# Optimization experiments

Hardware: AMD Instinct MI355X
Metric: run time of the kernel (lower is better)

## Reference

```python
import jax, jax.numpy as jnp
import numpy as np

N_USERS = 100000
N_ITEMS = 50000
N_NODES = N_USERS + N_ITEMS
N_EDGES = 4800000
EMB = 64
N_LAYERS = 3
BATCH = 16384


def setup_inputs() -> dict:
    key = jax.random.key(0)
    ks = jax.random.split(key, 12)
    users = jax.random.randint(ks[0], (BATCH,), 0, N_USERS)
    pos_items = jax.random.randint(ks[1], (BATCH,), 0, N_ITEMS)
    neg_items = jax.random.randint(ks[2], (BATCH,), 0, N_ITEMS)
    rows = jax.random.randint(ks[3], (N_EDGES,), 0, N_NODES)
    cols = jax.random.randint(ks[4], (N_EDGES,), 0, N_NODES)
    vals = jax.random.uniform(ks[5], (N_EDGES,), dtype=jnp.float32)
    # learned parameters (xavier-ish scale)
    user_emb = jax.random.normal(ks[6], (N_USERS, EMB), dtype=jnp.float32) * 0.1
    item_emb = jax.random.normal(ks[7], (N_ITEMS, EMB), dtype=jnp.float32) * 0.1
    # Linear weights stored as [in, out] so y = x @ W + b (matches torch Linear math)
    W1s = jax.random.normal(ks[8], (N_LAYERS, EMB, EMB), dtype=jnp.float32) * (1.0 / np.sqrt(EMB))
    b1s = jnp.zeros((N_LAYERS, EMB), dtype=jnp.float32)
    W2s = jax.random.normal(ks[9], (N_LAYERS, EMB, EMB), dtype=jnp.float32) * (1.0 / np.sqrt(EMB))
    b2s = jnp.zeros((N_LAYERS, EMB), dtype=jnp.float32)
    return dict(users=users, pos_items=pos_items, neg_items=neg_items,
                rows=rows, cols=cols, vals=vals,
                user_emb=user_emb, item_emb=item_emb,
                W1s=W1s, b1s=b1s, W2s=W2s, b2s=b2s)


def _leaky_relu(x):
    return jnp.where(x > 0, x, 0.2 * x)


def _computer(user_emb, item_emb, rows, cols, vals, W1s, b1s, W2s, b2s):
    all_emb = jnp.concatenate([user_emb, item_emb], axis=0)  # [N, 64]
    embs = [all_emb]
    for i in range(N_LAYERS):
        self_emb = all_emb @ W1s[i] + b1s[i]
        # sparse adjacency SpMM: gather neighbor features, weight, segment-sum by row
        neighbor = jax.ops.segment_sum(vals[:, None] * all_emb[cols], rows,
                                       num_segments=N_NODES)
        neighbor = neighbor @ W2s[i] + b2s[i]
        interact = (neighbor * all_emb) @ W2s[i] + b2s[i]
        all_emb = _leaky_relu(self_emb + neighbor + interact)
        embs.append(all_emb)
    embs = jnp.concatenate(embs, axis=1)  # [N, 64*(n_layers+1)] = [N, 256]
    return embs[:N_USERS], embs[N_USERS:]


def reference(users, pos_items, neg_items, rows, cols, vals,
              user_emb, item_emb, W1s, b1s, W2s, b2s):
    all_users, all_items = _computer(user_emb, item_emb, rows, cols, vals,
                                     W1s, b1s, W2s, b2s)
    users_emb = all_users[users]
    pos_emb = all_items[pos_items]
    neg_emb = all_items[neg_items]
    return users_emb, pos_emb, neg_emb
```

## Files before the change

kernel.cpp:

```cpp
#include <hip/hip_runtime.h>


#define EMB 64

constexpr int kNUsers = 100000;
constexpr int kNItems = 50000;
constexpr int kNNodes = 150000;
constexpr int kNEdges = 4800000;
constexpr int kBatch  = 16384;
constexpr int kLayers = 3;
constexpr int kRngShift = 8;
constexpr int kNRanges  = (kNNodes + 255) >> 8;
constexpr int kEdgesPerBin = 16384;
constexpr int kBinBlocks = (kNEdges + kEdgesPerBin - 1) / kEdgesPerBin;
constexpr int kEPW    = 16;

__device__ __forceinline__ float f4c(const float4& v, int i) {
  return ((const float*)&v)[i];
}
__device__ __forceinline__ float4 f4fma(float s, float4 w, float4 a) {
  a.x = fmaf(s, w.x, a.x);
  a.y = fmaf(s, w.y, a.y);
  a.z = fmaf(s, w.z, a.z);
  a.w = fmaf(s, w.w, a.w);
  return a;
}
__device__ __forceinline__ float4 f4add(float4 a, float4 b) {
  a.x += b.x; a.y += b.y; a.z += b.z; a.w += b.w;
  return a;
}
__device__ __forceinline__ float lrelu(float x) { return x > 0.f ? x : 0.2f * x; }
__device__ __forceinline__ unsigned short f2bf(float f) {
  unsigned int u = __float_as_uint(f);
  u = (u + 0x7fffu + ((u >> 16) & 1u)) >> 16;
  return (unsigned short)u;
}
__device__ __forceinline__ float bf2f(unsigned short h) {
  return __uint_as_float(((unsigned int)h) << 16);
}

#define F16(M) M(0) M(1) M(2) M(3) M(4) M(5) M(6) M(7) \
               M(8) M(9) M(10) M(11) M(12) M(13) M(14) M(15)

__global__ __launch_bounds__(256) void init_embed(
    const float* __restrict__ user_emb, const float* __restrict__ item_emb,
    float* __restrict__ cur, unsigned short* __restrict__ cur16, int with16)
{
  const size_t userF = (size_t)kNUsers * EMB;
  const size_t allF4 = (size_t)kNNodes * EMB / 4;
  const size_t i = (size_t)blockIdx.x * 256 + threadIdx.x;
  if (i >= allF4) return;
  const size_t f = i * 4;
  const float4 v = (f < userF) ? ((const float4*)user_emb)[i]
                               : ((const float4*)(item_emb))[(f - userF) / 4];
  ((float4*)cur)[i] = v;
  if (with16) {
    ushort4 h;
    h.x = f2bf(v.x); h.y = f2bf(v.y); h.z = f2bf(v.z); h.w = f2bf(v.w);
    ((ushort4*)cur16)[i] = h;
  }
}

__global__ __launch_bounds__(256) void refresh16(
    const float* __restrict__ cur, unsigned short* __restrict__ cur16)
{
  const size_t allF4 = (size_t)kNNodes * EMB / 4;
  const size_t i = (size_t)blockIdx.x * 256 + threadIdx.x;
  if (i >= allF4) return;
  const float4 v = ((const float4*)cur)[i];
  ushort4 h;
  h.x = f2bf(v.x); h.y = f2bf(v.y); h.z = f2bf(v.z); h.w = f2bf(v.w);
  ((ushort4*)cur16)[i] = h;
}


__global__ __launch_bounds__(1024) void hist_ranges(
    const int* __restrict__ rows, int* __restrict__ rangeA)
{
  __shared__ int cnt[kNRanges];
  const int tid = threadIdx.x;
  const int e0  = blockIdx.x * kEdgesPerBin;
  int e1 = e0 + kEdgesPerBin;
  if (e1 > kNEdges) e1 = kNEdges;
  for (int b = tid; b < kNRanges; b += 1024) cnt[b] = 0;
  __syncthreads();
  for (int e = e0 + tid; e < e1; e += 1024)
    atomicAdd(&cnt[rows[e] >> kRngShift], 1);
  __syncthreads();
  for (int b = tid; b < kNRanges; b += 1024)
    if (cnt[b] > 0) atomicAdd(&rangeA[b], cnt[b]);
}

__global__ __launch_bounds__(1024) void scan_ranges(
    int* __restrict__ rangeA, int* __restrict__ rowPtr)
{
  __shared__ int wsum[16];
  const int tid  = threadIdx.x;
  const int lane = tid & 63;
  const int wid  = tid >> 6;
  const int cnt  = (tid < kNRanges) ? rangeA[tid] : 0;
  int v = cnt;
#pragma unroll
  for (int off = 1; off < 64; off <<= 1) {
    const int n = __shfl_up(v, off, 64);
    if (lane >= off) v += n;
  }
  if (lane == 63) wsum[wid] = v;
  __syncthreads();
  if (tid == 0) {
    int s = 0;
#pragma unroll
    for (int w = 0; w < 16; ++w) { const int t = wsum[w]; wsum[w] = s; s += t; }
  }
  __syncthreads();
  if (tid < kNRanges) rangeA[tid] = wsum[wid] + v - cnt;
  if (tid == 0) {
    rangeA[kNRanges]  = kNEdges;
    rowPtr[kNNodes]   = kNEdges;
  }
}

__global__ __launch_bounds__(1024) void bin_edges(
    const int* __restrict__ rows, const int* __restrict__ cols,
    const float* __restrict__ vals, const int* __restrict__ rangeA,
    int* __restrict__ rangeCnt, int2* __restrict__ tmpE)
{
  __shared__ int cnt[kNRanges];
  __shared__ int base[kNRanges];
  const int tid = threadIdx.x;
  const int e0  = blockIdx.x * kEdgesPerBin;
  int e1 = e0 + kEdgesPerBin;
  if (e1 > kNEdges) e1 = kNEdges;

  for (int b = tid; b < kNRanges; b += 1024) cnt[b] = 0;
  __syncthreads();
  for (int e = e0 + tid; e < e1; e += 1024)
    atomicAdd(&cnt[rows[e] >> kRngShift], 1);
  __syncthreads();
  for (int b = tid; b < kNRanges; b += 1024) {
    const int c = cnt[b];
    base[b] = (c > 0) ? (rangeA[b] + atomicAdd(&rangeCnt[b], c)) : 0;
    cnt[b] = 0;
  }
  __syncthreads();
  for (int e = e0 + tid; e < e1; e += 1024) {
    const int r = rows[e];
    const int b = r >> kRngShift;
    const int rank = atomicAdd(&cnt[b], 1);
    tmpE[base[b] + rank] =
        make_int2(cols[e] | ((r & 255) << 18), __float_as_int(vals[e]));
  }
}

__global__ __launch_bounds__(256) void place_edges(
    const int2* __restrict__ tmpE, const int* __restrict__ rangeA,
    int2* __restrict__ edgeS, int* __restrict__ rowPtr)
{
  __shared__ int lcnt[256];
  __shared__ int lbase[256];
  __shared__ int ws[4];
  const int b    = blockIdx.x;
  const int r0   = b << kRngShift;
  const int tid  = threadIdx.x;
  const int lane = tid & 63;
  const int wid  = tid >> 6;
  const int start = rangeA[b];
  const int end   = rangeA[b + 1];

  lcnt[tid] = 0;
  __syncthreads();
  for (int e = start + tid; e < end; e += 256)
    atomicAdd(&lcnt[(tmpE[e].x >> 18) & 255], 1);
  __syncthreads();

  const int c = lcnt[tid];
  int v = c;
#pragma unroll
  for (int off = 1; off < 64; off <<= 1) {
    const int n = __shfl_up(v, off, 64);
    if (lane >= off) v += n;
  }
  if (lane == 63) ws[wid] = v;
  __syncthreads();
  int wadd = 0;
#pragma unroll
  for (int w = 0; w < 4; ++w) if (w < wid) wadd += ws[w];
  const int excl = v - c + wadd;
  lbase[tid] = start + excl;
  if (r0 + tid < kNNodes) rowPtr[r0 + tid] = start + excl;
  lcnt[tid] = 0;
  __syncthreads();

  for (int e = start + tid; e < end; e += 256) {
    const int2 cv = tmpE[e];
    const int rl  = (cv.x >> 18) & 255;
    const int rank = atomicAdd(&lcnt[rl], 1);
    edgeS[lbase[rl] + rank] = make_int2(cv.x & 0x3FFFF, cv.y);
  }
}

__global__ __launch_bounds__(256) void spmm_csr16f(
    const unsigned short* __restrict__ cur16, const int* __restrict__ rowPtr,
    const int2* __restrict__ edgeS, const float* __restrict__ W2,
    const float* __restrict__ b2, float* __restrict__ nbuf)
{
  const int lane = threadIdx.x & 63;
  const int r = (blockIdx.x << 2) | (threadIdx.x >> 6);
  if (r >= kNNodes) return;
  const int start = __builtin_amdgcn_readfirstlane(rowPtr[r]);
  const int end   = __builtin_amdgcn_readfirstlane(rowPtr[r + 1]);
  float a0 = 0.f, a1 = 0.f, a2 = 0.f, a3 = 0.f;
  int e = start;
  for (; e + 4 <= end; e += 4) {
    const int2 cv0 = edgeS[e];
    const int2 cv1 = edgeS[e + 1];
    const int2 cv2 = edgeS[e + 2];
    const int2 cv3 = edgeS[e + 3];
    const unsigned short u0 = cur16[(size_t)cv0.x * EMB + lane];
    const unsigned short u1 = cur16[(size_t)cv1.x * EMB + lane];
    const unsigned short u2 = cur16[(size_t)cv2.x * EMB + lane];
    const unsigned short u3 = cur16[(size_t)cv3.x * EMB + lane];
    a0 = fmaf(__int_as_float(cv0.y), bf2f(u0), a0);
    a1 = fmaf(__int_as_float(cv1.y), bf2f(u1), a1);
    a2 = fmaf(__int_as_float(cv2.y), bf2f(u2), a2);
    a3 = fmaf(__int_as_float(cv3.y), bf2f(u3), a3);
  }
  for (; e < end; ++e) {
    const int2 cv = edgeS[e];
    a0 = fmaf(__int_as_float(cv.y), bf2f(cur16[(size_t)cv.x * EMB + lane]), a0);
  }
  const float nsum = (a0 + a1) + (a2 + a3);

  float t = b2[lane];
#pragma unroll
  for (int k = 0; k < 64; ++k) {
    const float nk = __shfl(nsum, k, 64);
    t = fmaf(nk, W2[k * EMB + lane], t);
  }
  nbuf[(size_t)r * EMB + lane] = t;
}

__global__ __launch_bounds__(256) void spmm_csr(
    const float* __restrict__ cur, const int* __restrict__ rowPtr,
    const int2* __restrict__ edgeS, float* __restrict__ nbuf)
{
  const int lane = threadIdx.x & 63;
  const int r = (blockIdx.x << 2) | (threadIdx.x >> 6);
  if (r >= kNNodes) return;
  const int start = __builtin_amdgcn_readfirstlane(rowPtr[r]);
  const int end   = __builtin_amdgcn_readfirstlane(rowPtr[r + 1]);
  float a0 = 0.f, a1 = 0.f, a2 = 0.f, a3 = 0.f;
  int e = start;
  for (; e + 4 <= end; e += 4) {
    const int2 cv0 = edgeS[e];
    const int2 cv1 = edgeS[e + 1];
    const int2 cv2 = edgeS[e + 2];
    const int2 cv3 = edgeS[e + 3];
    a0 = fmaf(__int_as_float(cv0.y), cur[(size_t)cv0.x * EMB + lane], a0);
    a1 = fmaf(__int_as_float(cv1.y), cur[(size_t)cv1.x * EMB + lane], a1);
    a2 = fmaf(__int_as_float(cv2.y), cur[(size_t)cv2.x * EMB + lane], a2);
    a3 = fmaf(__int_as_float(cv3.y), cur[(size_t)cv3.x * EMB + lane], a3);
  }
  for (; e < end; ++e) {
    const int2 cv = edgeS[e];
    a0 = fmaf(__int_as_float(cv.y), cur[(size_t)cv.x * EMB + lane], a0);
  }
  nbuf[(size_t)r * EMB + lane] = (a0 + a1) + (a2 + a3);
}

__global__ __launch_bounds__(256) void spmm_atomic(
    const float* __restrict__ cur, const int* __restrict__ rows,
    const int* __restrict__ cols, const float* __restrict__ vals,
    float* __restrict__ nbuf)
{
  const int lane = threadIdx.x & 63;
  int wv = (blockIdx.x << 2) | (threadIdx.x >> 6);
  wv = __builtin_amdgcn_readfirstlane(wv);
  int e0 = wv * kEPW;
  int e1 = e0 + kEPW;
  if (e1 > kNEdges) e1 = kNEdges;
  for (int e = e0; e < e1; ++e) {
    atomicAdd(nbuf + (size_t)rows[e] * EMB + lane,
              vals[e] * cur[(size_t)cols[e] * EMB + lane]);
  }
}

__global__ __launch_bounds__(256) void transform_nbr(
    float* __restrict__ nbuf, const float* __restrict__ W2,
    const float* __restrict__ b2)
{
  const int node = blockIdx.x * 256 + threadIdx.x;
  if (node >= kNNodes) return;
  const float4* __restrict__ nr  = (const float4*)(nbuf + (size_t)node * EMB);
  const float4* __restrict__ b2v = (const float4*)b2;
#define DECL(j) float4 a##j = b2v[j];
  F16(DECL)
#undef DECL
#pragma unroll 4
  for (int k4 = 0; k4 < 16; ++k4) {
    const float4 nv = nr[k4];
#pragma unroll
    for (int kk = 0; kk < 4; ++kk) {
      const float ns = f4c(nv, kk);
      const float4* __restrict__ w2r = (const float4*)(W2 + (4 * k4 + kk) * EMB);
#define STEP(j) a##j = f4fma(ns, w2r[j], a##j);
      F16(STEP)
#undef STEP
    }
  }
  float4* __restrict__ outp = (float4*)(nbuf + (size_t)node * EMB);
#define STORE(j) outp[j] = a##j;
  F16(STORE)
#undef STORE
}

__global__ __launch_bounds__(256) void transform_self(
    float* __restrict__ cur, const float* __restrict__ nbuf,
    const float* __restrict__ W1, const float* __restrict__ b1,
    const float* __restrict__ b2, const float* __restrict__ W2)
{
  const int node = blockIdx.x * 256 + threadIdx.x;
  if (node >= kNNodes) return;
  const float4* __restrict__ xr  = (const float4*)(cur  + (size_t)node * EMB);
  const float4* __restrict__ tr  = (const float4*)(nbuf + (size_t)node * EMB);
  const float4* __restrict__ b1v = (const float4*)b1;
  const float4* __restrict__ b2v = (const float4*)b2;
#define DECL(j) float4 a##j = f4add(b1v[j], b2v[j]);
  F16(DECL)
#undef DECL
#pragma unroll 2
  for (int k4 = 0; k4 < 16; ++k4) {
    const float4 xv = xr[k4];
    const float4 tv = tr[k4];
#pragma unroll
    for (int kk = 0; kk < 4; ++kk) {
      const float xs = f4c(xv, kk);
      const float ms = f4c(tv, kk) * xs;
      const int k = 4 * k4 + kk;
      const float4* __restrict__ w1r = (const float4*)(W1 + k * EMB);
      const float4* __restrict__ w2r = (const float4*)(W2 + k * EMB);
#define STEP(j) a##j = f4fma(xs, w1r[j], a##j); a##j = f4fma(ms, w2r[j], a##j);
      F16(STEP)
#undef STEP
    }
  }
  float4* __restrict__ outp = (float4*)(cur + (size_t)node * EMB);
#define STORE(j) { const float4 tj = tr[j]; float4 r;          \
    r.x = lrelu(a##j.x + tj.x); r.y = lrelu(a##j.y + tj.y);    \
    r.z = lrelu(a##j.z + tj.z); r.w = lrelu(a##j.w + tj.w);    \
    outp[j] = r; }
  F16(STORE)
#undef STORE
}

__global__ __launch_bounds__(256) void gather_out(
    const float* __restrict__ cur, const int* __restrict__ users,
    const int* __restrict__ pos, const int* __restrict__ neg,
    float* __restrict__ out, int layer)
{
  const int t    = blockIdx.x * 256 + threadIdx.x;
  const int lane = t & 63;
  const int rid  = t >> 6;
  if (rid >= 3 * kBatch) return;
  const int seg = rid / kBatch;
  const int b   = rid - seg * kBatch;
  int idx;
  if (seg == 0)      idx = users[b];
  else if (seg == 1) idx = pos[b] + kNUsers;
  else               idx = neg[b] + kNUsers;
  out[(size_t)rid * 256 + layer * EMB + lane] = cur[(size_t)idx * EMB + lane];
}

extern "C" void kernel_launch(void* const* d_in, const int* in_sizes, int n_in,
                              void* d_out, int out_size, void* d_ws, size_t ws_size,
                              hipStream_t stream) {
  const int*   users    = (const int*)d_in[0];
  const int*   pos      = (const int*)d_in[1];
  const int*   neg      = (const int*)d_in[2];
  const int*   rows     = (const int*)d_in[3];
  const int*   cols     = (const int*)d_in[4];
  const float* vals     = (const float*)d_in[5];
  const float* user_emb = (const float*)d_in[6];
  const float* item_emb = (const float*)d_in[7];
  const float* W1s      = (const float*)d_in[8];
  const float* b1s      = (const float*)d_in[9];
  const float* W2s      = (const float*)d_in[10];
  const float* b2s      = (const float*)d_in[11];
  float* out = (float*)d_out;

  const size_t nodeF = (size_t)kNNodes * EMB;
  float* cur  = (float*)d_ws;
  float* nbuf = cur + nodeF;
  int2*  edgeS     = (int2*)(nbuf + nodeF);
  int*   rowPtr    = (int*)(edgeS + kNEdges);
  int*   rangeA    = rowPtr + (kNNodes + 1);
  int*   rangeCnt  = rangeA + (kNRanges + 1);
  unsigned short* cur16 = (unsigned short*)(rangeCnt + kNRanges);
  int2*  tmpE = (int2*)nbuf;
  const size_t neededCsr = (size_t)((char*)cur16 - (char*)d_ws);
  const size_t needed16  = neededCsr + nodeF * sizeof(unsigned short);
  const bool useCsr = ws_size >= neededCsr;
  const bool use16  = useCsr && ws_size >= needed16;

  const dim3 blk(256);
  const int iblocks = (int)((nodeF / 4 + 255) / 256);
  const int gblocks = (3 * kBatch * EMB + 255) / 256;
  const int rblocks = (kNNodes + 3) / 4;
  const int tblocks = (kNNodes + 255) / 256;

  init_embed<<<iblocks, blk, 0, stream>>>(user_emb, item_emb, cur, cur16,
                                          use16 ? 1 : 0);

  if (useCsr) {
    hipMemsetAsync(rangeA, 0, (size_t)(2 * kNRanges + 1) * sizeof(int), stream);
    hist_ranges<<<kBinBlocks, dim3(1024), 0, stream>>>(rows, rangeA);
    scan_ranges<<<1, 1024, 0, stream>>>(rangeA, rowPtr);
    bin_edges<<<kBinBlocks, dim3(1024), 0, stream>>>(rows, cols, vals, rangeA,
                                                     rangeCnt, tmpE);
    place_edges<<<kNRanges, blk, 0, stream>>>(tmpE, rangeA, edgeS, rowPtr);
  }

  gather_out<<<gblocks, blk, 0, stream>>>(cur, users, pos, neg, out, 0);

  for (int L = 0; L < kLayers; ++L) {
    const float* W1 = W1s + L * EMB * EMB;
    const float* b1 = b1s + L * EMB;
    const float* W2 = W2s + L * EMB * EMB;
    const float* b2 = b2s + L * EMB;
    if (useCsr && use16) {
      spmm_csr16f<<<rblocks, blk, 0, stream>>>(cur16, rowPtr, edgeS, W2, b2,
                                               nbuf);
    } else if (useCsr) {
      spmm_csr<<<rblocks, blk, 0, stream>>>(cur, rowPtr, edgeS, nbuf);
      transform_nbr<<<tblocks, blk, 0, stream>>>(nbuf, W2, b2);
    } else {
      hipMemsetAsync(nbuf, 0, nodeF * sizeof(float), stream);
      const int sblocks = (((kNEdges + kEPW - 1) / kEPW) + 3) / 4;
      spmm_atomic<<<sblocks, blk, 0, stream>>>(cur, rows, cols, vals, nbuf);
      transform_nbr<<<tblocks, blk, 0, stream>>>(nbuf, W2, b2);
    }
    transform_self<<<tblocks, blk, 0, stream>>>(cur, nbuf, W1, b1, b2, W2);
    if (use16 && L + 1 < kLayers)
      refresh16<<<iblocks, blk, 0, stream>>>(cur, cur16);
    gather_out<<<gblocks, blk, 0, stream>>>(cur, users, pos, neg, out, L + 1);
  }
}
```

Before: 1.177 ms.

## Stage binned edges in shared memory for coalesced scatter; split W2 accumulator chain

The edge-binning kernel now processes 4096-edge sub-blocks. Each sub-block computes local ranks, prefix-sums the per-range counts, and sorts its records into shared memory, so the writes to tmpE become contiguous runs per range instead of scattered 8-byte stores. This adds shared-memory use and more barriers per sub-block. Separately, the per-row 64x64 W2 product in the fused SpMM kernel now uses four independent accumulators to shorten the FMA dependency chain.

```diff
diff --git a/kernel.cpp b/kernel.cpp
--- a/kernel.cpp
+++ b/kernel.cpp
@@ -13,6 +13,7 @@
 constexpr int kNRanges  = (kNNodes + 255) >> 8;
 constexpr int kEdgesPerBin = 16384;
 constexpr int kBinBlocks = (kNEdges + kEdgesPerBin - 1) / kEdgesPerBin;
+constexpr int kSub    = 4096;
 constexpr int kEPW    = 16;
 
 __device__ __forceinline__ float f4c(const float4& v, int i) {
@@ -126,29 +127,78 @@
     int* __restrict__ rangeCnt, int2* __restrict__ tmpE)
 {
   __shared__ int cnt[kNRanges];
-  __shared__ int base[kNRanges];
-  const int tid = threadIdx.x;
-  const int e0  = blockIdx.x * kEdgesPerBin;
+  __shared__ int lofs[kNRanges];
+  __shared__ int gbase[kNRanges];
+  __shared__ int wsum[16];
+  __shared__ int2 sbuf[kSub];
+  __shared__ unsigned short grg[kSub];
+  const int tid  = threadIdx.x;
+  const int lane = tid & 63;
+  const int wid  = tid >> 6;
+  const int e0   = blockIdx.x * kEdgesPerBin;
   int e1 = e0 + kEdgesPerBin;
   if (e1 > kNEdges) e1 = kNEdges;
 
-  for (int b = tid; b < kNRanges; b += 1024) cnt[b] = 0;
-  __syncthreads();
-  for (int e = e0 + tid; e < e1; e += 1024)
-    atomicAdd(&cnt[rows[e] >> kRngShift], 1);
-  __syncthreads();
-  for (int b = tid; b < kNRanges; b += 1024) {
-    const int c = cnt[b];
-    base[b] = (c > 0) ? (rangeA[b] + atomicAdd(&rangeCnt[b], c)) : 0;
-    cnt[b] = 0;
-  }
-  __syncthreads();
-  for (int e = e0 + tid; e < e1; e += 1024) {
-    const int r = rows[e];
-    const int b = r >> kRngShift;
-    const int rank = atomicAdd(&cnt[b], 1);
-    tmpE[base[b] + rank] =
-        make_int2(cols[e] | ((r & 255) << 18), __float_as_int(vals[e]));
+  for (int sb = e0; sb < e1; sb += kSub) {
+    const int n = min(kSub, e1 - sb);
+    for (int g = tid; g < kNRanges; g += 1024) cnt[g] = 0;
+    __syncthreads();
+
+    int  myg[4], myrank[4];
+    int2 myrec[4];
+#pragma unroll
+    for (int k = 0; k < 4; ++k) {
+      const int i = k * 1024 + tid;
+      myg[k] = -1;
+      if (i < n) {
+        const int e = sb + i;
+        const int r = rows[e];
+        const int g = r >> kRngShift;
+        myg[k]    = g;
+        myrank[k] = atomicAdd(&cnt[g], 1);
+        myrec[k]  = make_int2(cols[e] | ((r & 255) << 18),
+                              __float_as_int(vals[e]));
+      }
+    }
+    __syncthreads();
+
+    const int c = (tid < kNRanges) ? cnt[tid] : 0;
+    int v = c;
+#pragma unroll
+    for (int off = 1; off < 64; off <<= 1) {
+      const int x = __shfl_up(v, off, 64);
+      if (lane >= off) v += x;
+    }
+    if (lane == 63) wsum[wid] = v;
+    __syncthreads();
+    if (tid == 0) {
+      int s = 0;
+#pragma unroll
+      for (int w = 0; w < 16; ++w) { const int t = wsum[w]; wsum[w] = s; s += t; }
+    }
+    __syncthreads();
+    if (tid < kNRanges) {
+      const int excl = wsum[wid] + v - c;
+      lofs[tid] = excl;
+      gbase[tid] = (c > 0) ? (rangeA[tid] + atomicAdd(&rangeCnt[tid], c)) : 0;
+    }
+    __syncthreads();
+
+#pragma unroll
+    for (int k = 0; k < 4; ++k) {
+      if (myg[k] >= 0) {
+        const int slot = lofs[myg[k]] + myrank[k];
+        sbuf[slot] = myrec[k];
+        grg[slot]  = (unsigned short)myg[k];
+      }
+    }
+    __syncthreads();
+
+    for (int t = tid; t < n; t += 1024) {
+      const int g = grg[t];
+      tmpE[gbase[g] + (t - lofs[g])] = sbuf[t];
+    }
+    __syncthreads();
   }
 }
 
@@ -231,13 +281,19 @@
   }
   const float nsum = (a0 + a1) + (a2 + a3);
 
-  float t = b2[lane];
-#pragma unroll
-  for (int k = 0; k < 64; ++k) {
-    const float nk = __shfl(nsum, k, 64);
-    t = fmaf(nk, W2[k * EMB + lane], t);
-  }
-  nbuf[(size_t)r * EMB + lane] = t;
+  float t0 = b2[lane], t1 = 0.f, t2 = 0.f, t3 = 0.f;
+#pragma unroll
+  for (int k = 0; k < 64; k += 4) {
+    const float nk0 = __shfl(nsum, k,     64);
+    const float nk1 = __shfl(nsum, k + 1, 64);
+    const float nk2 = __shfl(nsum, k + 2, 64);
+    const float nk3 = __shfl(nsum, k + 3, 64);
+    t0 = fmaf(nk0, W2[(k    ) * EMB + lane], t0);
+    t1 = fmaf(nk1, W2[(k + 1) * EMB + lane], t1);
+    t2 = fmaf(nk2, W2[(k + 2) * EMB + lane], t2);
+    t3 = fmaf(nk3, W2[(k + 3) * EMB + lane], t3);
+  }
+  nbuf[(size_t)r * EMB + lane] = (t0 + t1) + (t2 + t3);
 }
 
 __global__ __launch_bounds__(256) void spmm_csr(
```

New measurement: 1.163 ms. No clear change (-1.2%).
